# Kernel optimization log

Hardware: AMD Instinct MI355X
Metric: run time of the kernel (lower is better)

The kernel has to match this reference:

```python
import jax, jax.numpy as jnp
import numpy as np

K = 16  # centroids per codebook (4-bit LUT indices, blink-mm convention)


def _im2col(x, kh, kw, stride, pad):
    # x: [B, C, H, W] -> [B, P, C*kh*kw] with channel-major feature ordering
    # (each length-(kh*kw) subvector is one channel's patch, matching the
    #  per-channel codebook layout of the 3x3 AMM conv).
    B, C, H, W = x.shape
    xp = jnp.pad(x, ((0, 0), (0, 0), (pad, pad), (pad, pad)))
    Ho = (H + 2 * pad - kh) // stride + 1
    Wo = (W + 2 * pad - kw) // stride + 1
    cols = [xp[:, :, i:i + stride * Ho:stride, j:j + stride * Wo:stride]
            for i in range(kh) for j in range(kw)]  # fixed small loop (<=9)
    feat = jnp.stack(cols, axis=2)                      # [B, C, kh*kw, Ho, Wo]
    feat = feat.reshape(B, C * kh * kw, Ho, Wo)
    feat = feat.transpose(0, 2, 3, 1).reshape(B, Ho * Wo, C * kh * kw)
    return feat, Ho, Wo


def _amm_conv_bn_act(x, centroids, lut, scale, bias, kernel, stride, pad, relu):
    # Product-quantization approximate matmul conv:
    #  1) im2col, split feature dim D into ncodebooks subspaces of dim dsub
    #  2) nearest-centroid (L2) assignment per subspace -> 4-bit index
    #  3) gather+accumulate precomputed LUT dot products over codebooks
    #  4) folded BatchNorm affine + optional ReLU
    feat, Ho, Wo = _im2col(x, kernel, kernel, stride, pad)
    B, P, D = feat.shape
    ncb, k, dsub = centroids.shape
    xs = feat.reshape(B, P, ncb, dsub)
    dots = jnp.einsum('bpcd,ckd->bpck', xs, centroids)          # [B,P,ncb,K]
    c2 = jnp.sum(centroids * centroids, axis=-1)                # [ncb,K]
    idx = jnp.argmin(c2[None, None] - 2.0 * dots, axis=-1)      # [B,P,ncb]
    onehot = jax.nn.one_hot(idx, k, dtype=x.dtype)              # [B,P,ncb,K]
    out = jnp.einsum('bpck,cko->bpo', onehot, lut)              # LUT accumulate
    out = out * scale + bias                                    # folded BN
    if relu:
        out = jax.nn.relu(out)
    Cout = lut.shape[-1]
    return out.reshape(B, Ho, Wo, Cout).transpose(0, 3, 1, 2)


def setup_inputs() -> dict:
    key = jax.random.key(0)
    ks = jax.random.split(key, 16)
    inplanes, planes, width = 1024, 256, 256
    B, H, W = 32, 14, 14
    d = {}
    d['x'] = jax.random.normal(ks[0], (B, inplanes, H, W), dtype=jnp.float32)
    d['c1_centroids'] = jax.random.normal(ks[1], (inplanes // 4, K, 4), dtype=jnp.float32)
    d['c1_lut'] = jax.random.normal(ks[2], (inplanes // 4, K, width), dtype=jnp.float32) * 0.1
    d['c1_scale'] = jax.random.uniform(ks[3], (width,), dtype=jnp.float32, minval=0.5, maxval=1.5)
    d['c1_bias'] = jax.random.normal(ks[4], (width,), dtype=jnp.float32) * 0.1
    d['c2_centroids'] = jax.random.normal(ks[5], (width, K, 9), dtype=jnp.float32)
    d['c2_lut'] = jax.random.normal(ks[6], (width, K, width), dtype=jnp.float32) * 0.1
    d['c2_scale'] = jax.random.uniform(ks[7], (width,), dtype=jnp.float32, minval=0.5, maxval=1.5)
    d['c2_bias'] = jax.random.normal(ks[8], (width,), dtype=jnp.float32) * 0.1
    d['c3_centroids'] = jax.random.normal(ks[9], (width // 4, K, 4), dtype=jnp.float32)
    d['c3_lut'] = jax.random.normal(ks[10], (width // 4, K, planes * 4), dtype=jnp.float32) * 0.1
    d['c3_scale'] = jax.random.uniform(ks[11], (planes * 4,), dtype=jnp.float32, minval=0.5, maxval=1.5)
    d['c3_bias'] = jax.random.normal(ks[12], (planes * 4,), dtype=jnp.float32) * 0.1
    return d


def reference(x, c1_centroids, c1_lut, c1_scale, c1_bias,
              c2_centroids, c2_lut, c2_scale, c2_bias,
              c3_centroids, c3_lut, c3_scale, c3_bias):
    identity = x
    out = _amm_conv_bn_act(x, c1_centroids, c1_lut, c1_scale, c1_bias,
                           kernel=1, stride=1, pad=0, relu=True)
    out = _amm_conv_bn_act(out, c2_centroids, c2_lut, c2_scale, c2_bias,
                           kernel=3, stride=1, pad=1, relu=True)
    out = _amm_conv_bn_act(out, c3_centroids, c3_lut, c3_scale, c3_bias,
                           kernel=1, stride=1, pad=0, relu=False)
    # QuantizedAdd + QuantizedReLU (float reference math: add then relu)
    return jax.nn.relu(out + identity)
```

## Files before the change

kernel.cpp:

```cpp
#include <hip/hip_runtime.h>
#include <stdint.h>

#define PP 196
#define BP 6272


template <typename T>
__global__ __launch_bounds__(256) void assign_1x1(
    const T* __restrict__ in, const float* __restrict__ cents,
    uint32_t* __restrict__ idxp, int nchan) {
  __shared__ double s_cent[8][16][4];
  __shared__ double s_c2[8][16];
  const int chunk = blockIdx.y;
  const int t = threadIdx.x;
  for (int i = t; i < 8 * 16 * 4; i += 256)
    ((double*)s_cent)[i] = (double)cents[(size_t)chunk * 512 + i];
  __syncthreads();
  if (t < 128) {
    int cb_l = t >> 4, k = t & 15;
    double s = 0.0;
#pragma unroll
    for (int d = 0; d < 4; d++) { double c = s_cent[cb_l][k][d]; s += c * c; }
    s_c2[cb_l][k] = s;
  }
  __syncthreads();
  const int p = blockIdx.x * 256 + t;
  if (p >= BP) return;
  const unsigned b = (unsigned)p / 196u;
  const unsigned pr = (unsigned)p - b * 196u;
  const T* xb = in + ((size_t)b * nchan + chunk * 32) * PP + pr;
  double xv[32];
#pragma unroll
  for (int i = 0; i < 32; i++) xv[i] = (double)xb[(size_t)i * PP];
  uint32_t word = 0;
#pragma unroll
  for (int cb_l = 0; cb_l < 8; cb_l++) {
    double best = 1e300; int bi = 0;
#pragma unroll
    for (int k = 0; k < 16; k++) {
      double dot = 0.0;
#pragma unroll
      for (int d = 0; d < 4; d++) dot = fma(xv[cb_l * 4 + d], s_cent[cb_l][k][d], dot);
      double dist = s_c2[cb_l][k] - 2.0 * dot;
      if (dist < best) { best = dist; bi = k; }
    }
    word |= (uint32_t)bi << (4 * cb_l);
  }
  idxp[(size_t)chunk * BP + p] = word;
}

__global__ __launch_bounds__(256) void assign_3x3(
    const double* __restrict__ in, const float* __restrict__ cents,
    uint32_t* __restrict__ idxp) {
  __shared__ double s_cent[8][16][9];
  __shared__ double s_c2[8][16];
  const int chunk = blockIdx.y;
  const int c0 = chunk * 8;
  const int t = threadIdx.x;
  for (int i = t; i < 8 * 16 * 9; i += 256)
    ((double*)s_cent)[i] = (double)cents[(size_t)c0 * 144 + i];
  __syncthreads();
  if (t < 128) {
    int cb_l = t >> 4, k = t & 15;
    double s = 0.0;
#pragma unroll
    for (int d = 0; d < 9; d++) { double c = s_cent[cb_l][k][d]; s += c * c; }
    s_c2[cb_l][k] = s;
  }
  __syncthreads();
  const int p = blockIdx.x * 256 + t;
  if (p >= BP) return;
  const unsigned b = (unsigned)p / 196u;
  const unsigned pr = (unsigned)p - b * 196u;
  const int oh = pr / 14, ow = pr - oh * 14;
  uint32_t word = 0;
  for (int cb_l = 0; cb_l < 8; cb_l++) {
    const double* base = in + ((size_t)b * 256 + (c0 + cb_l)) * PP;
    double v[9];
#pragma unroll
    for (int i = 0; i < 3; i++) {
#pragma unroll
      for (int j = 0; j < 3; j++) {
        int hh = oh + i - 1, ww = ow + j - 1;
        bool ok = (hh >= 0) & (hh < 14) & (ww >= 0) & (ww < 14);
        v[i * 3 + j] = ok ? base[hh * 14 + ww] : 0.0;
      }
    }
    double best = 1e300; int bi = 0;
#pragma unroll
    for (int k = 0; k < 16; k++) {
      double dot = 0.0;
#pragma unroll
      for (int d = 0; d < 9; d++) dot = fma(v[d], s_cent[cb_l][k][d], dot);
      double dist = s_c2[cb_l][k] - 2.0 * dot;
      if (dist < best) { best = dist; bi = k; }
    }
    word |= (uint32_t)bi << (4 * cb_l);
  }
  idxp[(size_t)chunk * BP + p] = word;
}

template <int NCB, int NOUT, bool RELU, bool RES, typename OutT>
__global__ __launch_bounds__(512) void accum_kernel(
    const float* __restrict__ lut, const uint32_t* __restrict__ idxp,
    const float* __restrict__ scale, const float* __restrict__ bias,
    const float* __restrict__ res, OutT* __restrict__ out) {
  __shared__ float s_lut[16 * 16 * 36];
  const int t = threadIdx.x;
  const int lane = t & 63;
  const int wave = t >> 6;
  const int oquad = wave & 3;
  const int pg = wave >> 2;
  const int p = blockIdx.x * 128 + pg * 64 + lane;
  const int o_base = blockIdx.y * 16;
  const int r = t >> 1, h = t & 1;
  const int cb_ls = r >> 4, ks = r & 15;
  double a0 = 0.0, a1 = 0.0, a2 = 0.0, a3 = 0.0;
  constexpr int NCHUNK = NCB / 16;
  for (int ch = 0; ch < NCHUNK; ch++) {
    __syncthreads();
    uint32_t w0 = idxp[(size_t)(ch * 2) * BP + p];
    uint32_t w1 = idxp[(size_t)(ch * 2 + 1) * BP + p];
    {
      const float* g = lut + (((size_t)(ch * 16 + cb_ls)) * 16 + ks) * NOUT + o_base + h * 8;
      float4 va = *(const float4*)g;
      float4 vb = *(const float4*)(g + 4);
      float* sd = s_lut + cb_ls * 576 + ks * 36 + h * 8;
      *(float4*)sd = va;
      *(float4*)(sd + 4) = vb;
    }
    __syncthreads();
#pragma unroll
    for (int cb_l = 0; cb_l < 16; cb_l++) {
      uint32_t w = (cb_l < 8) ? w0 : w1;
      int idx = (int)((w >> (4 * (cb_l & 7))) & 15u);
      const float4 v = *(const float4*)(s_lut + cb_l * 576 + idx * 36 + oquad * 4);
      a0 += (double)v.x; a1 += (double)v.y; a2 += (double)v.z; a3 += (double)v.w;
    }
  }
  const unsigned b = (unsigned)p / 196u;
  const unsigned pr = (unsigned)p - b * 196u;
  const int o = o_base + oquad * 4;
  const float4 sc = *(const float4*)(scale + o);
  const float4 bs = *(const float4*)(bias + o);
  double r0 = a0 * (double)sc.x + (double)bs.x;
  double r1 = a1 * (double)sc.y + (double)bs.y;
  double r2 = a2 * (double)sc.z + (double)bs.z;
  double r3 = a3 * (double)sc.w + (double)bs.w;
  if (RES) {
    const float* rp = res + ((size_t)b * NOUT + o) * PP + pr;
    r0 += (double)rp[0 * PP]; r1 += (double)rp[1 * PP];
    r2 += (double)rp[2 * PP]; r3 += (double)rp[3 * PP];
  }
  if (RELU) {
    r0 = fmax(r0, 0.0); r1 = fmax(r1, 0.0);
    r2 = fmax(r2, 0.0); r3 = fmax(r3, 0.0);
  }
  OutT* op = out + ((size_t)b * NOUT + o) * PP + pr;
  op[0 * PP] = (OutT)r0; op[1 * PP] = (OutT)r1;
  op[2 * PP] = (OutT)r2; op[3 * PP] = (OutT)r3;
}


extern "C" void kernel_launch(void* const* d_in, const int* in_sizes, int n_in,
                              void* d_out, int out_size, void* d_ws, size_t ws_size,
                              hipStream_t stream) {
  const float* x   = (const float*)d_in[0];
  const float* c1c = (const float*)d_in[1];
  const float* c1l = (const float*)d_in[2];
  const float* c1s = (const float*)d_in[3];
  const float* c1b = (const float*)d_in[4];
  const float* c2c = (const float*)d_in[5];
  const float* c2l = (const float*)d_in[6];
  const float* c2s = (const float*)d_in[7];
  const float* c2b = (const float*)d_in[8];
  const float* c3c = (const float*)d_in[9];
  const float* c3l = (const float*)d_in[10];
  const float* c3s = (const float*)d_in[11];
  const float* c3b = (const float*)d_in[12];

  const size_t sz_i1 = (size_t)32 * BP * 4;
  const size_t sz_i2 = (size_t)32 * BP * 4;
  const size_t sz_i3 = (size_t)8 * BP * 4;
  const size_t sz_o64 = (size_t)BP * 256 * 8;

  char* w = (char*)d_ws;
  uint32_t* i1 = (uint32_t*)w; w += sz_i1;
  uint32_t* i2 = (uint32_t*)w; w += sz_i2;
  uint32_t* i3 = (uint32_t*)w; w += sz_i3;
  double *out1, *out2;
  if (ws_size >= sz_i1 + sz_i2 + sz_i3 + 2 * sz_o64) {
    out1 = (double*)w;
    out2 = (double*)(w + sz_o64);
  } else {
    out1 = (double*)d_out;
    out2 = out1 + (size_t)BP * 256;
  }

  const dim3 blkA(256), blkC(512);
  assign_1x1<float><<<dim3(25, 32), blkA, 0, stream>>>(x, c1c, i1, 1024);
  accum_kernel<256, 256, true, false, double><<<dim3(49, 16), blkC, 0, stream>>>(
      c1l, i1, c1s, c1b, nullptr, out1);
  assign_3x3<<<dim3(25, 32), blkA, 0, stream>>>(out1, c2c, i2);
  accum_kernel<256, 256, true, false, double><<<dim3(49, 16), blkC, 0, stream>>>(
      c2l, i2, c2s, c2b, nullptr, out2);
  assign_1x1<double><<<dim3(25, 8), blkA, 0, stream>>>(out2, c3c, i3, 256);
  accum_kernel<64, 1024, true, true, float><<<dim3(49, 64), blkC, 0, stream>>>(
      c3l, i3, c3s, c3b, x, (float*)d_out);
}
```

Baseline: 274.9 us.

## Use fp32 centroid search with fp64 fallback and fp16 LUT accumulate for conv3

The centroid-assignment kernels now compute distances in fp32 and only redo the wave's search in fp64 when the best and second-best distances are within a small margin, avoiding most double-precision work. The final conv's LUT accumulation moves to a new kernel that converts LUT entries to fp16 in shared memory and sums them with packed half2 adds, flushing to fp32 every eight codebooks. This trades exactness for throughput. Near-ties below the margin could still flip indices, and fp16 LUT values and partial sums add rounding error to the output.

```diff
diff --git a/kernel.cpp b/kernel.cpp
--- a/kernel.cpp
+++ b/kernel.cpp
@@ -3,25 +3,33 @@
 
 #define PP 196
 #define BP 6272
+
+typedef _Float16 half_t;
+typedef half_t half8v __attribute__((ext_vector_type(8)));
+typedef half_t half2v __attribute__((ext_vector_type(2)));
 
 
 template <typename T>
 __global__ __launch_bounds__(256) void assign_1x1(
     const T* __restrict__ in, const float* __restrict__ cents,
     uint32_t* __restrict__ idxp, int nchan) {
-  __shared__ double s_cent[8][16][4];
-  __shared__ double s_c2[8][16];
+  __shared__ float  sf[8][16][4];
+  __shared__ double sd[8][16][6];
   const int chunk = blockIdx.y;
   const int t = threadIdx.x;
-  for (int i = t; i < 8 * 16 * 4; i += 256)
-    ((double*)s_cent)[i] = (double)cents[(size_t)chunk * 512 + i];
+  for (int i = t; i < 512; i += 256) {
+    float c = cents[(size_t)chunk * 512 + i];
+    int cb = i >> 6, r = i & 63;
+    sf[cb][r >> 2][r & 3] = c;
+    sd[cb][r >> 2][1 + (r & 3)] = (double)c;
+  }
   __syncthreads();
   if (t < 128) {
-    int cb_l = t >> 4, k = t & 15;
+    int cb = t >> 4, k = t & 15;
     double s = 0.0;
 #pragma unroll
-    for (int d = 0; d < 4; d++) { double c = s_cent[cb_l][k][d]; s += c * c; }
-    s_c2[cb_l][k] = s;
+    for (int d = 0; d < 4; d++) { double c = sd[cb][k][1 + d]; s += c * c; }
+    sd[cb][k][0] = s;
   }
   __syncthreads();
   const int p = blockIdx.x * 256 + t;
@@ -29,22 +37,42 @@
   const unsigned b = (unsigned)p / 196u;
   const unsigned pr = (unsigned)p - b * 196u;
   const T* xb = in + ((size_t)b * nchan + chunk * 32) * PP + pr;
-  double xv[32];
-#pragma unroll
-  for (int i = 0; i < 32; i++) xv[i] = (double)xb[(size_t)i * PP];
+  T xr[32];
+#pragma unroll
+  for (int i = 0; i < 32; i++) xr[i] = xb[(size_t)i * PP];
+  float xs2[32];
+#pragma unroll
+  for (int i = 0; i < 32; i++) xs2[i] = 2.f * (float)xr[i];
   uint32_t word = 0;
-#pragma unroll
-  for (int cb_l = 0; cb_l < 8; cb_l++) {
-    double best = 1e300; int bi = 0;
+#pragma unroll 1
+  for (int cb = 0; cb < 8; cb++) {
+    float best = 1e30f, sec = 1e30f; int bi = 0;
 #pragma unroll
     for (int k = 0; k < 16; k++) {
-      double dot = 0.0;
-#pragma unroll
-      for (int d = 0; d < 4; d++) dot = fma(xv[cb_l * 4 + d], s_cent[cb_l][k][d], dot);
-      double dist = s_c2[cb_l][k] - 2.0 * dot;
-      if (dist < best) { best = dist; bi = k; }
-    }
-    word |= (uint32_t)bi << (4 * cb_l);
+      const float4 c = *(const float4*)&sf[cb][k][0];
+      float dist = c.x * (c.x - xs2[cb * 4 + 0]);
+      dist = fmaf(c.y, c.y - xs2[cb * 4 + 1], dist);
+      dist = fmaf(c.z, c.z - xs2[cb * 4 + 2], dist);
+      dist = fmaf(c.w, c.w - xs2[cb * 4 + 3], dist);
+      if (dist < best) { sec = best; best = dist; bi = k; }
+      else sec = fminf(sec, dist);
+    }
+    if (__any(sec - best < 2e-4f)) {
+      double xv[4];
+#pragma unroll
+      for (int d = 0; d < 4; d++) xv[d] = (double)xr[cb * 4 + d];
+      double bb = 1e300; int bi64 = 0;
+#pragma unroll
+      for (int k = 0; k < 16; k++) {
+        double dot = 0.0;
+#pragma unroll
+        for (int d = 0; d < 4; d++) dot = fma(xv[d], sd[cb][k][1 + d], dot);
+        double dist = sd[cb][k][0] - 2.0 * dot;
+        if (dist < bb) { bb = dist; bi64 = k; }
+      }
+      bi = bi64;
+    }
+    word |= (uint32_t)bi << (4 * cb);
   }
   idxp[(size_t)chunk * BP + p] = word;
 }
@@ -52,20 +80,30 @@
 __global__ __launch_bounds__(256) void assign_3x3(
     const double* __restrict__ in, const float* __restrict__ cents,
     uint32_t* __restrict__ idxp) {
-  __shared__ double s_cent[8][16][9];
-  __shared__ double s_c2[8][16];
+  __shared__ float  sf[8][16][12];
+  __shared__ double sd[8][16][10];
   const int chunk = blockIdx.y;
-  const int c0 = chunk * 8;
+  const int c0g = chunk * 8;
   const int t = threadIdx.x;
-  for (int i = t; i < 8 * 16 * 9; i += 256)
-    ((double*)s_cent)[i] = (double)cents[(size_t)c0 * 144 + i];
+  for (int i = t; i < 1152; i += 256) {
+    int cb = i / 144, r = i - cb * 144;
+    int k = r / 9, d = r - k * 9;
+    float c = cents[(size_t)(c0g + cb) * 144 + k * 9 + d];
+    sf[cb][k][1 + d] = c;
+    sd[cb][k][1 + d] = (double)c;
+  }
   __syncthreads();
   if (t < 128) {
-    int cb_l = t >> 4, k = t & 15;
+    int cb = t >> 4, k = t & 15;
     double s = 0.0;
-#pragma unroll
-    for (int d = 0; d < 9; d++) { double c = s_cent[cb_l][k][d]; s += c * c; }
-    s_c2[cb_l][k] = s;
+    float s32 = 0.f;
+#pragma unroll
+    for (int d = 0; d < 9; d++) {
+      double c = sd[cb][k][1 + d]; s += c * c;
+      float cf = sf[cb][k][1 + d]; s32 += cf * cf;
+    }
+    sd[cb][k][0] = s;
+    sf[cb][k][0] = s32;
   }
   __syncthreads();
   const int p = blockIdx.x * 256 + t;
@@ -74,34 +112,59 @@
   const unsigned pr = (unsigned)p - b * 196u;
   const int oh = pr / 14, ow = pr - oh * 14;
   uint32_t word = 0;
-  for (int cb_l = 0; cb_l < 8; cb_l++) {
-    const double* base = in + ((size_t)b * 256 + (c0 + cb_l)) * PP;
-    double v[9];
-#pragma unroll
-    for (int i = 0; i < 3; i++) {
-#pragma unroll
-      for (int j = 0; j < 3; j++) {
-        int hh = oh + i - 1, ww = ow + j - 1;
+#pragma unroll 1
+  for (int cb = 0; cb < 8; cb++) {
+    const double* base = in + ((size_t)b * 256 + (c0g + cb)) * PP;
+    double v64[9]; float v32[9];
+#pragma unroll
+    for (int r = 0; r < 3; r++) {
+#pragma unroll
+      for (int cc = 0; cc < 3; cc++) {
+        int hh = oh + r - 1, ww = ow + cc - 1;
         bool ok = (hh >= 0) & (hh < 14) & (ww >= 0) & (ww < 14);
-        v[i * 3 + j] = ok ? base[hh * 14 + ww] : 0.0;
+        double v = ok ? base[hh * 14 + ww] : 0.0;
+        v64[r * 3 + cc] = v;
+        v32[r * 3 + cc] = (float)v;
       }
     }
-    double best = 1e300; int bi = 0;
+    float best = 1e30f, sec = 1e30f; int bi = 0;
 #pragma unroll
     for (int k = 0; k < 16; k++) {
-      double dot = 0.0;
-#pragma unroll
-      for (int d = 0; d < 9; d++) dot = fma(v[d], s_cent[cb_l][k][d], dot);
-      double dist = s_c2[cb_l][k] - 2.0 * dot;
-      if (dist < best) { best = dist; bi = k; }
-    }
-    word |= (uint32_t)bi << (4 * cb_l);
+      const float4 cA = *(const float4*)&sf[cb][k][0];
+      const float4 cB = *(const float4*)&sf[cb][k][4];
+      const float4 cC = *(const float4*)&sf[cb][k][8];
+      float dot = v32[0] * cA.y;
+      dot = fmaf(v32[1], cA.z, dot);
+      dot = fmaf(v32[2], cA.w, dot);
+      dot = fmaf(v32[3], cB.x, dot);
+      dot = fmaf(v32[4], cB.y, dot);
+      dot = fmaf(v32[5], cB.z, dot);
+      dot = fmaf(v32[6], cB.w, dot);
+      dot = fmaf(v32[7], cC.x, dot);
+      dot = fmaf(v32[8], cC.y, dot);
+      float dist = fmaf(-2.f, dot, cA.x);
+      if (dist < best) { sec = best; best = dist; bi = k; }
+      else sec = fminf(sec, dist);
+    }
+    if (__any(sec - best < 4e-4f)) {
+      double bb = 1e300; int bi64 = 0;
+#pragma unroll
+      for (int k = 0; k < 16; k++) {
+        double dot = 0.0;
+#pragma unroll
+        for (int d = 0; d < 9; d++) dot = fma(v64[d], sd[cb][k][1 + d], dot);
+        double dist = sd[cb][k][0] - 2.0 * dot;
+        if (dist < bb) { bb = dist; bi64 = k; }
+      }
+      bi = bi64;
+    }
+    word |= (uint32_t)bi << (4 * cb);
   }
   idxp[(size_t)chunk * BP + p] = word;
 }
 
 template <int NCB, int NOUT, bool RELU, bool RES, typename OutT>
-__global__ __launch_bounds__(512) void accum_kernel(
+__global__ __launch_bounds__(512) void accum_f64(
     const float* __restrict__ lut, const uint32_t* __restrict__ idxp,
     const float* __restrict__ scale, const float* __restrict__ bias,
     const float* __restrict__ res, OutT* __restrict__ out) {
@@ -109,13 +172,13 @@
   const int t = threadIdx.x;
   const int lane = t & 63;
   const int wave = t >> 6;
-  const int oquad = wave & 3;
+  const int q = wave & 3;
   const int pg = wave >> 2;
   const int p = blockIdx.x * 128 + pg * 64 + lane;
   const int o_base = blockIdx.y * 16;
   const int r = t >> 1, h = t & 1;
   const int cb_ls = r >> 4, ks = r & 15;
-  double a0 = 0.0, a1 = 0.0, a2 = 0.0, a3 = 0.0;
+  double a0 = 0, a1 = 0, a2 = 0, a3 = 0;
   constexpr int NCHUNK = NCB / 16;
   for (int ch = 0; ch < NCHUNK; ch++) {
     __syncthreads();
@@ -125,22 +188,22 @@
       const float* g = lut + (((size_t)(ch * 16 + cb_ls)) * 16 + ks) * NOUT + o_base + h * 8;
       float4 va = *(const float4*)g;
       float4 vb = *(const float4*)(g + 4);
-      float* sd = s_lut + cb_ls * 576 + ks * 36 + h * 8;
-      *(float4*)sd = va;
-      *(float4*)(sd + 4) = vb;
+      float* sdm = s_lut + cb_ls * 576 + ks * 36 + h * 8;
+      *(float4*)sdm = va;
+      *(float4*)(sdm + 4) = vb;
     }
     __syncthreads();
 #pragma unroll
     for (int cb_l = 0; cb_l < 16; cb_l++) {
       uint32_t w = (cb_l < 8) ? w0 : w1;
       int idx = (int)((w >> (4 * (cb_l & 7))) & 15u);
-      const float4 v = *(const float4*)(s_lut + cb_l * 576 + idx * 36 + oquad * 4);
+      const float4 v = *(const float4*)(s_lut + cb_l * 576 + idx * 36 + q * 4);
       a0 += (double)v.x; a1 += (double)v.y; a2 += (double)v.z; a3 += (double)v.w;
     }
   }
   const unsigned b = (unsigned)p / 196u;
   const unsigned pr = (unsigned)p - b * 196u;
-  const int o = o_base + oquad * 4;
+  const int o = o_base + q * 4;
   const float4 sc = *(const float4*)(scale + o);
   const float4 bs = *(const float4*)(bias + o);
   double r0 = a0 * (double)sc.x + (double)bs.x;
@@ -159,6 +222,76 @@
   OutT* op = out + ((size_t)b * NOUT + o) * PP + pr;
   op[0 * PP] = (OutT)r0; op[1 * PP] = (OutT)r1;
   op[2 * PP] = (OutT)r2; op[3 * PP] = (OutT)r3;
+}
+
+__global__ __launch_bounds__(256) void accum3_f16(
+    const float* __restrict__ lut, const uint32_t* __restrict__ idxp,
+    const float* __restrict__ scale, const float* __restrict__ bias,
+    const float* __restrict__ res, float* __restrict__ out) {
+  __shared__ half_t s16[16 * 640];
+  const int t = threadIdx.x;
+  const int lane = t & 63;
+  const int wave = t >> 6;
+  const int h = wave & 1;
+  const int pg = wave >> 1;
+  const int p = blockIdx.x * 128 + pg * 64 + lane;
+  const int o_base = blockIdx.y * 16;
+  const int s0 = t, s1 = t + 256;
+  const int cA = s0 >> 5, kA = (s0 >> 1) & 15, hA = s0 & 1;
+  const int cB = s1 >> 5, kB = (s1 >> 1) & 15, hB = s1 & 1;
+  const size_t cs = (size_t)16 * 16 * 1024;
+  constexpr int NCHUNK = 4;
+  float acc[8];
+#pragma unroll
+  for (int i = 0; i < 8; i++) acc[i] = 0.f;
+  for (int ch = 0; ch < NCHUNK; ch++) {
+    __syncthreads();
+    uint32_t w0 = idxp[(size_t)(ch * 2) * BP + p];
+    uint32_t w1 = idxp[(size_t)(ch * 2 + 1) * BP + p];
+    {
+      const float* gA = lut + (size_t)ch * cs + ((size_t)cA * 16 + kA) * 1024 + o_base + hA * 8;
+      const float* gB = lut + (size_t)ch * cs + ((size_t)cB * 16 + kB) * 1024 + o_base + hB * 8;
+      float4 a0 = *(const float4*)gA;
+      float4 a1 = *(const float4*)(gA + 4);
+      float4 b0 = *(const float4*)gB;
+      float4 b1 = *(const float4*)(gB + 4);
+      half8v va, vb;
+      va[0] = (half_t)a0.x; va[1] = (half_t)a0.y; va[2] = (half_t)a0.z; va[3] = (half_t)a0.w;
+      va[4] = (half_t)a1.x; va[5] = (half_t)a1.y; va[6] = (half_t)a1.z; va[7] = (half_t)a1.w;
+      vb[0] = (half_t)b0.x; vb[1] = (half_t)b0.y; vb[2] = (half_t)b0.z; vb[3] = (half_t)b0.w;
+      vb[4] = (half_t)b1.x; vb[5] = (half_t)b1.y; vb[6] = (half_t)b1.z; vb[7] = (half_t)b1.w;
+      *(half8v*)(s16 + cA * 640 + kA * 40 + hA * 8) = va;
+      *(half8v*)(s16 + cB * 640 + kB * 40 + hB * 8) = vb;
+    }
+    __syncthreads();
+#pragma unroll
+    for (int half_grp = 0; half_grp < 2; half_grp++) {
+      half2v p0 = 0, p1 = 0, p2 = 0, p3 = 0;
+      uint32_t w = half_grp ? w1 : w0;
+#pragma unroll
+      for (int j = 0; j < 8; j++) {
+        int cb_l = half_grp * 8 + j;
+        int idx = (int)((w >> (4 * j)) & 15u);
+        const half8v v = *(const half8v*)(s16 + cb_l * 640 + idx * 40 + h * 8);
+        const half2v* vp = (const half2v*)&v;
+        p0 += vp[0]; p1 += vp[1]; p2 += vp[2]; p3 += vp[3];
+      }
+      acc[0] += (float)p0[0]; acc[1] += (float)p0[1];
+      acc[2] += (float)p1[0]; acc[3] += (float)p1[1];
+      acc[4] += (float)p2[0]; acc[5] += (float)p2[1];
+      acc[6] += (float)p3[0]; acc[7] += (float)p3[1];
+    }
+  }
+  const unsigned b = (unsigned)p / 196u;
+  const unsigned pr = (unsigned)p - b * 196u;
+  const int o = o_base + h * 8;
+  const float* rp = res + ((size_t)b * 1024 + o) * PP + pr;
+  float* op = out + ((size_t)b * 1024 + o) * PP + pr;
+#pragma unroll
+  for (int i = 0; i < 8; i++) {
+    float v = acc[i] * scale[o + i] + bias[o + i] + rp[(size_t)i * PP];
+    op[(size_t)i * PP] = fmaxf(v, 0.f);
+  }
 }
 
 
@@ -189,7 +322,7 @@
   uint32_t* i2 = (uint32_t*)w; w += sz_i2;
   uint32_t* i3 = (uint32_t*)w; w += sz_i3;
   double *out1, *out2;
-  if (ws_size >= sz_i1 + sz_i2 + sz_i3 + 2 * sz_o64) {
+  if (ws_size >= (size_t)(w - (char*)d_ws) + 2 * sz_o64) {
     out1 = (double*)w;
     out2 = (double*)(w + sz_o64);
   } else {
@@ -197,14 +330,14 @@
     out2 = out1 + (size_t)BP * 256;
   }
 
-  const dim3 blkA(256), blkC(512);
+  const dim3 blkA(256);
   assign_1x1<float><<<dim3(25, 32), blkA, 0, stream>>>(x, c1c, i1, 1024);
-  accum_kernel<256, 256, true, false, double><<<dim3(49, 16), blkC, 0, stream>>>(
+  accum_f64<256, 256, true, false, double><<<dim3(49, 16), dim3(512), 0, stream>>>(
       c1l, i1, c1s, c1b, nullptr, out1);
   assign_3x3<<<dim3(25, 32), blkA, 0, stream>>>(out1, c2c, i2);
-  accum_kernel<256, 256, true, false, double><<<dim3(49, 16), blkC, 0, stream>>>(
+  accum_f64<256, 256, true, false, double><<<dim3(49, 16), dim3(512), 0, stream>>>(
       c2l, i2, c2s, c2b, nullptr, out2);
   assign_1x1<double><<<dim3(25, 8), blkA, 0, stream>>>(out2, c3c, i3, 256);
-  accum_kernel<64, 1024, true, true, float><<<dim3(49, 64), blkC, 0, stream>>>(
+  accum3_f16<<<dim3(49, 64), blkA, 0, stream>>>(
       c3l, i3, c3s, c3b, x, (float*)d_out);
 }
```

New measurement: 266.4 us. -3.1%, faster.
